# Kernel tuning notes

Hardware: AMD Instinct MI355X
Metric: run time of the kernel (lower is better)

## Reference

```python
import jax, jax.numpy as jnp
import numpy as np

N = 32768      # nodes
E = 262144     # edges (avg degree 8)
D = 128        # d_model (= per-head out_channels, concat=False)
H = 4          # heads
C = D          # out_channels per head
R = 64         # rel_dim (edge_dim)
NREL = 64      # n_rels
L = 2          # num_layers
LEAK = 0.2     # GATv2 leaky_relu slope
LN_EPS = 1e-5


def setup_inputs() -> dict:
    key = jax.random.key(0)
    ks = jax.random.split(key, 12)
    sdD = 1.0 / np.sqrt(D)
    sdR = 1.0 / np.sqrt(R)
    return {
        "x_flat": jax.random.normal(ks[0], (N, D), jnp.float32),
        "edge_index": jax.random.randint(ks[1], (2, E), 0, N, jnp.int64),
        "edge_type": jax.random.randint(ks[2], (E,), 0, NREL, jnp.int64),
        "valid_mask_flat": jnp.ones((N,), bool),
        "rel_emb": jax.random.normal(ks[3], (NREL, R), jnp.float32) * 0.1,
        "Wl": jax.random.normal(ks[4], (L, D, H * C), jnp.float32) * sdD,
        "bl": jnp.zeros((L, H * C), jnp.float32),
        "Wr": jax.random.normal(ks[5], (L, D, H * C), jnp.float32) * sdD,
        "br": jnp.zeros((L, H * C), jnp.float32),
        "We": jax.random.normal(ks[6], (L, R, H * C), jnp.float32) * sdR,
        "att": jax.random.normal(ks[7], (L, H, C), jnp.float32) * 0.1,
        "bias_o": jnp.zeros((L, D), jnp.float32),
        "ln_g": jnp.ones((L, D), jnp.float32),
        "ln_b": jnp.zeros((L, D), jnp.float32),
    }


def _gatv2_layer(h, src, dst, ea, Wl, bl, Wr, br, We, att, b):
    # h: [N,D]; src/dst: [E+N]; ea: [E+N,R] edge embeddings (incl. self loops)
    xl = (h @ Wl + bl).reshape(N, H, C)   # source transform
    xr = (h @ Wr + br).reshape(N, H, C)   # target transform
    ep = (ea @ We).reshape(-1, H, C)
    e = jax.nn.leaky_relu(xl[src] + xr[dst] + ep, LEAK)   # [E+N,H,C]
    logits = jnp.einsum('ehc,hc->eh', e, att)             # [E+N,H]
    # segment softmax over destination node
    m = jax.ops.segment_max(logits, dst, num_segments=N)
    m = jnp.where(jnp.isfinite(m), m, 0.0)
    p = jnp.exp(logits - m[dst])
    denom = jax.ops.segment_sum(p, dst, num_segments=N)
    alpha = p / (denom[dst] + 1e-16)                      # [E+N,H]
    out = jax.ops.segment_sum(alpha[:, :, None] * xl[src], dst, num_segments=N)
    return out.mean(axis=1) + b                           # concat=False -> head mean


def reference(x_flat, edge_index, edge_type, valid_mask_flat,
              rel_emb, Wl, bl, Wr, br, We, att, bias_o, ln_g, ln_b):
    x = jnp.where(valid_mask_flat[:, None], x_flat, 0.0)
    src, dst = edge_index[0], edge_index[1]
    ea = rel_emb[edge_type]                               # [E,R]
    # PyG add_self_loops with fill_value='mean': self-loop edge_attr is the
    # mean of incoming edge attrs per target node (0 if no incoming edges).
    ones = jnp.ones((E,), x.dtype)
    deg = jax.ops.segment_sum(ones, dst, num_segments=N)
    self_attr = jax.ops.segment_sum(ea, dst, num_segments=N) / jnp.maximum(deg, 1.0)[:, None]
    loop = jnp.arange(N, dtype=src.dtype)
    src_f = jnp.concatenate([src, loop])
    dst_f = jnp.concatenate([dst, loop])
    ea_f = jnp.concatenate([ea, self_attr], axis=0)

    h = x
    for l in range(L):
        msg = _gatv2_layer(h, src_f, dst_f, ea_f,
                           Wl[l], bl[l], Wr[l], br[l], We[l], att[l], bias_o[l])
        msg = jax.nn.gelu(msg, approximate=False)         # dropout = identity (eval)
        hn = h + msg
        mu = jnp.mean(hn, axis=-1, keepdims=True)
        var = jnp.mean(jnp.square(hn - mu), axis=-1, keepdims=True)
        h = (hn - mu) / jnp.sqrt(var + LN_EPS) * ln_g[l] + ln_b[l]
    return jnp.where(valid_mask_flat[:, None], h, 0.0)
```

## Files before the change

kernel.cpp:

```cpp
#include <hip/hip_runtime.h>
#include <hip/hip_bf16.h>
#include <math.h>

#define NN 32768
#define EE 262144
#define DM 128
#define HH 4
#define CC 128
#define HC 512
#define RD 64
#define NRELS 64
#define LEAKS 0.2f
#define LNEPS 1e-5f

typedef __hip_bfloat16 bf16;
typedef __attribute__((ext_vector_type(8))) short short8;
typedef __attribute__((ext_vector_type(4))) float f32x4;

__device__ __forceinline__ void unpack8(uint4 u, float* f) {
    f[0] = __uint_as_float((u.x & 0xffffu) << 16);
    f[1] = __uint_as_float(u.x & 0xffff0000u);
    f[2] = __uint_as_float((u.y & 0xffffu) << 16);
    f[3] = __uint_as_float(u.y & 0xffff0000u);
    f[4] = __uint_as_float((u.z & 0xffffu) << 16);
    f[5] = __uint_as_float(u.z & 0xffff0000u);
    f[6] = __uint_as_float((u.w & 0xffffu) << 16);
    f[7] = __uint_as_float(u.w & 0xffff0000u);
}

__global__ void k_deg(const int* __restrict__ dst, int* __restrict__ deg) {
    int e = blockIdx.x * 1024 + threadIdx.x;
    atomicAdd(&deg[dst[e]], 1);
}

__global__ void k_scan1(const int* __restrict__ deg, int* __restrict__ rowptr,
                        int* __restrict__ bsum) {
    __shared__ int s[256];
    int b = blockIdx.x, t = threadIdx.x;
    int v = deg[b * 256 + t];
    s[t] = v;
    __syncthreads();
    for (int off = 1; off < 256; off <<= 1) {
        int x = (t >= off) ? s[t - off] : 0;
        __syncthreads();
        s[t] += x;
        __syncthreads();
    }
    rowptr[b * 256 + t] = s[t] - v;
    if (t == 255) bsum[b] = s[255];
}

__global__ void k_small(const int* __restrict__ bsum, int* __restrict__ boff,
                        const int* __restrict__ hist, int* __restrict__ bcur) {
    __shared__ int s[128];
    int t = threadIdx.x;
    if (blockIdx.x == 0) {
        if (t < 128) {
            int v = bsum[t];
            s[t] = v;
        }
        __syncthreads();
        for (int off = 1; off < 128; off <<= 1) {
            int x = (t >= off && t < 128) ? s[t - off] : 0;
            __syncthreads();
            if (t < 128) s[t] += x;
            __syncthreads();
        }
        if (t < 128) boff[t] = s[t] - bsum[t];
        if (t == 127) boff[128] = s[127];
    } else {
        if (t < 64) s[t] = hist[t];
        __syncthreads();
        for (int off = 1; off < 64; off <<= 1) {
            int x = (t >= off && t < 64) ? s[t - off] : 0;
            __syncthreads();
            if (t < 64) s[t] += x;
            __syncthreads();
        }
        if (t < 64) bcur[t] = s[t] - hist[t];
    }
}

__global__ void k_s3p(int* __restrict__ rowptr, const int* __restrict__ boff,
                      const int* __restrict__ deg, int* __restrict__ bcur,
                      int* __restrict__ perm) {
    __shared__ int lh[64], lbase[64];
    int t = threadIdx.x;
    int i = blockIdx.x * 256 + t;
    rowptr[i] += boff[i >> 8];
    if (i == NN - 1) rowptr[NN] = boff[128];
    if (t < 64) lh[t] = 0;
    __syncthreads();
    int d = deg[i];
    int b = 63 - (d > 63 ? 63 : d);
    int my = atomicAdd(&lh[b], 1);
    __syncthreads();
    if (t < 64 && lh[t] > 0) lbase[t] = atomicAdd(&bcur[t], lh[t]);
    __syncthreads();
    perm[lbase[b] + my] = i;
}

__global__ void k_hist(const int* __restrict__ deg, int* __restrict__ hist) {
    __shared__ int lh[64];
    int t = threadIdx.x;
    if (t < 64) lh[t] = 0;
    __syncthreads();
    int d = deg[blockIdx.x * 256 + t];
    int b = 63 - (d > 63 ? 63 : d);
    atomicAdd(&lh[b], 1);
    __syncthreads();
    if (t < 64 && lh[t] > 0) atomicAdd(&hist[t], lh[t]);
}

__global__ void k_fill(const int* __restrict__ src, const int* __restrict__ dst,
                       const int* __restrict__ etype, const int* __restrict__ rowptr,
                       int* __restrict__ cursor, unsigned* __restrict__ csr) {
    int e = blockIdx.x * 1024 + threadIdx.x;
    int d = dst[e];
    int pos = atomicAdd(&cursor[d], 1);
    csr[rowptr[d] + pos] = (unsigned)src[e] | ((unsigned)etype[e] << 16);
}

__global__ void k_prep(const float* __restrict__ x, bf16* __restrict__ hb,
                       const float* __restrict__ Wl, const float* __restrict__ Wr,
                       bf16* __restrict__ Wt,
                       const float* __restrict__ rel_emb, const float* __restrict__ We,
                       bf16* __restrict__ wep) {
    __shared__ float sa[RD];
    int b = blockIdx.x, tid = threadIdx.x;
    if (b < 2048) {
        int i = b * 256 + tid;
        const float4* p = (const float4*)x;
        float4 f0 = p[i * 2], f1 = p[i * 2 + 1];
        bf16 o[8];
        o[0] = __float2bfloat16(f0.x); o[1] = __float2bfloat16(f0.y);
        o[2] = __float2bfloat16(f0.z); o[3] = __float2bfloat16(f0.w);
        o[4] = __float2bfloat16(f1.x); o[5] = __float2bfloat16(f1.y);
        o[6] = __float2bfloat16(f1.z); o[7] = __float2bfloat16(f1.w);
        *reinterpret_cast<uint4*>(hb + (size_t)i * 8) = *reinterpret_cast<uint4*>(o);
    } else if (b < 3072) {
        int idx = (b - 2048) * 256 + tid;
        int l = idx >> 17;
        int rem = idx & 131071;
        int k = rem >> 10;
        int c = rem & 1023;
        const float* WlL = Wl + (size_t)l * DM * HC;
        const float* WrL = Wr + (size_t)l * DM * HC;
        float v = (c < HC) ? WlL[k * HC + c] : WrL[k * HC + (c - HC)];
        Wt[(size_t)l * 1024 * DM + (size_t)c * DM + k] = __float2bfloat16(v);
    } else {
        int blk = b - 3072;
        int l = blk >> 6, r = blk & 63;
        const float* WeL = We + (size_t)l * RD * HC;
        if (tid < RD) sa[tid] = rel_emb[r * RD + tid];
        __syncthreads();
        for (int c = tid; c < HC; c += 256) {
            float s = 0.f;
#pragma unroll 8
            for (int k = 0; k < RD; ++k) s += sa[k] * WeL[k * HC + c];
            wep[(size_t)l * NRELS * HC + (size_t)r * HC + c] = __float2bfloat16(s);
        }
    }
}

__global__ __launch_bounds__(256) void k_gemm_mfma(
    const bf16* __restrict__ hb, const bf16* __restrict__ Wt,
    const float* __restrict__ bl, const float* __restrict__ br,
    bf16* __restrict__ xlb, bf16* __restrict__ xrb) {
    int lane = threadIdx.x & 63;
    int wave = threadIdx.x >> 6;
    int rbase = blockIdx.x * 32;
    int lr = lane & 15;
    int lk = lane >> 4;
    const short* ha = (const short*)hb;
    const short* wa = (const short*)Wt;

    short8 a[2][4];
#pragma unroll
    for (int mi = 0; mi < 2; ++mi)
#pragma unroll
        for (int kk = 0; kk < 4; ++kk)
            a[mi][kk] = *(const short8*)(ha + (size_t)(rbase + mi * 16 + lr) * DM + kk * 32 + lk * 8);

    for (int cg = 0; cg < 4; ++cg) {
        int cbase = cg * 256 + wave * 64;
        short8 b[4][4];
#pragma unroll
        for (int ni = 0; ni < 4; ++ni)
#pragma unroll
            for (int kk = 0; kk < 4; ++kk)
                b[ni][kk] = *(const short8*)(wa + (size_t)(cbase + ni * 16 + lr) * DM + kk * 32 + lk * 8);

        f32x4 c[2][4];
#pragma unroll
        for (int mi = 0; mi < 2; ++mi)
#pragma unroll
            for (int ni = 0; ni < 4; ++ni)
                c[mi][ni] = (f32x4){0.f, 0.f, 0.f, 0.f};

#pragma unroll
        for (int kk = 0; kk < 4; ++kk)
#pragma unroll
            for (int mi = 0; mi < 2; ++mi)
#pragma unroll
                for (int ni = 0; ni < 4; ++ni)
                    c[mi][ni] = __builtin_amdgcn_mfma_f32_16x16x32_bf16(
                        a[mi][kk], b[ni][kk], c[mi][ni], 0, 0, 0);

#pragma unroll
        for (int ni = 0; ni < 4; ++ni) {
            int col = cbase + ni * 16 + lr;
            float bv = (col < HC) ? bl[col] : br[col - HC];
            bf16* outp;
            int cc;
            if (col < HC) { outp = xlb; cc = col; } else { outp = xrb; cc = col - HC; }
#pragma unroll
            for (int mi = 0; mi < 2; ++mi) {
#pragma unroll
                for (int r = 0; r < 4; ++r) {
                    int row = rbase + mi * 16 + lk * 4 + r;
                    outp[(size_t)row * HC + cc] = __float2bfloat16(c[mi][ni][r] + bv);
                }
            }
        }
    }
}

__global__ void k_node(
    const bf16* __restrict__ xlb, const bf16* __restrict__ xrb,
    const bf16* __restrict__ wep,
    const unsigned* __restrict__ csr, const int* __restrict__ rowptr,
    const int* __restrict__ perm,
    const float* __restrict__ attL, const float* __restrict__ biasL,
    const float* __restrict__ lngL, const float* __restrict__ lnbL,
    const float* __restrict__ h_in, float* __restrict__ h_out,
    bf16* __restrict__ hb_out) {
    int tid = threadIdx.x;
    int lane = tid & 63;
    int wave = tid >> 6;
    int n = perm[blockIdx.x * 4 + wave];
    int head = lane >> 4;
    const int g0 = lane * 8;
    const int ch0 = (lane & 15) * 8;
    const short* xla = (const short*)xlb;
    const short* wpa = (const short*)wep;

    float attv[8];
#pragma unroll
    for (int j = 0; j < 8; ++j) attv[j] = attL[head * CC + ch0 + j];

    float xrn[8];
    unpack8(*(const uint4*)((const short*)xrb + (size_t)n * HC + g0), xrn);

    const float4* hp = (const float4*)(h_in + (size_t)n * DM + ch0);
    float4 h0 = hp[0], h1 = hp[1];

    float denom = 0.f;
    float acc[8], wpsum[8];
#pragma unroll
    for (int j = 0; j < 8; ++j) { acc[j] = 0.f; wpsum[j] = 0.f; }

    int r0 = rowptr[n], r1 = rowptr[n + 1];
    int d = r1 - r0;

    int i = r0;
    for (; i + 3 < r1; i += 4) {
        unsigned u0 = csr[i], u1 = csr[i + 1], u2 = csr[i + 2], u3 = csr[i + 3];
        uint4 xv0 = *(const uint4*)(xla + (size_t)(u0 & 0xffffu) * HC + g0);
        uint4 xv1 = *(const uint4*)(xla + (size_t)(u1 & 0xffffu) * HC + g0);
        uint4 xv2 = *(const uint4*)(xla + (size_t)(u2 & 0xffffu) * HC + g0);
        uint4 xv3 = *(const uint4*)(xla + (size_t)(u3 & 0xffffu) * HC + g0);
        uint4 wv0 = *(const uint4*)(wpa + (size_t)(u0 >> 16) * HC + g0);
        uint4 wv1 = *(const uint4*)(wpa + (size_t)(u1 >> 16) * HC + g0);
        uint4 wv2 = *(const uint4*)(wpa + (size_t)(u2 >> 16) * HC + g0);
        uint4 wv3 = *(const uint4*)(wpa + (size_t)(u3 >> 16) * HC + g0);
        float xs0[8], xs1[8], xs2[8], xs3[8];
        float w0[8], w1[8], w2[8], w3[8];
        unpack8(xv0, xs0); unpack8(xv1, xs1);
        unpack8(xv2, xs2); unpack8(xv3, xs3);
        unpack8(wv0, w0); unpack8(wv1, w1);
        unpack8(wv2, w2); unpack8(wv3, w3);
        float p0 = 0.f, p1 = 0.f, p2 = 0.f, p3 = 0.f;
#pragma unroll
        for (int j = 0; j < 8; ++j) {
            wpsum[j] += (w0[j] + w1[j]) + (w2[j] + w3[j]);
            float v0 = xs0[j] + xrn[j] + w0[j];
            v0 = (v0 > 0.f) ? v0 : LEAKS * v0;
            p0 += v0 * attv[j];
            float v1 = xs1[j] + xrn[j] + w1[j];
            v1 = (v1 > 0.f) ? v1 : LEAKS * v1;
            p1 += v1 * attv[j];
            float v2 = xs2[j] + xrn[j] + w2[j];
            v2 = (v2 > 0.f) ? v2 : LEAKS * v2;
            p2 += v2 * attv[j];
            float v3 = xs3[j] + xrn[j] + w3[j];
            v3 = (v3 > 0.f) ? v3 : LEAKS * v3;
            p3 += v3 * attv[j];
        }
        p0 += __shfl_xor(p0, 1); p1 += __shfl_xor(p1, 1);
        p2 += __shfl_xor(p2, 1); p3 += __shfl_xor(p3, 1);
        p0 += __shfl_xor(p0, 2); p1 += __shfl_xor(p1, 2);
        p2 += __shfl_xor(p2, 2); p3 += __shfl_xor(p3, 2);
        p0 += __shfl_xor(p0, 4); p1 += __shfl_xor(p1, 4);
        p2 += __shfl_xor(p2, 4); p3 += __shfl_xor(p3, 4);
        p0 += __shfl_xor(p0, 8); p1 += __shfl_xor(p1, 8);
        p2 += __shfl_xor(p2, 8); p3 += __shfl_xor(p3, 8);

        float e0 = __expf(fminf(p0, 80.f));
        float e1 = __expf(fminf(p1, 80.f));
        float e2 = __expf(fminf(p2, 80.f));
        float e3 = __expf(fminf(p3, 80.f));
        denom += (e0 + e1) + (e2 + e3);
#pragma unroll
        for (int j = 0; j < 8; ++j)
            acc[j] += (e0 * xs0[j] + e1 * xs1[j]) + (e2 * xs2[j] + e3 * xs3[j]);
    }
    for (; i < r1; ++i) {
        unsigned u = csr[i];
        uint4 xv = *(const uint4*)(xla + (size_t)(u & 0xffffu) * HC + g0);
        uint4 wv = *(const uint4*)(wpa + (size_t)(u >> 16) * HC + g0);
        float xs[8], wp[8];
        unpack8(xv, xs);
        unpack8(wv, wp);
        float p2 = 0.f;
#pragma unroll
        for (int j = 0; j < 8; ++j) {
            wpsum[j] += wp[j];
            float v = xs[j] + xrn[j] + wp[j];
            v = (v > 0.f) ? v : LEAKS * v;
            p2 += v * attv[j];
        }
        p2 += __shfl_xor(p2, 1);
        p2 += __shfl_xor(p2, 2);
        p2 += __shfl_xor(p2, 4);
        p2 += __shfl_xor(p2, 8);
        float pe = __expf(fminf(p2, 80.f));
        denom += pe;
#pragma unroll
        for (int j = 0; j < 8; ++j) acc[j] += pe * xs[j];
    }

    float xln[8];
    unpack8(*(const uint4*)(xla + (size_t)n * HC + g0), xln);
    float invd = (d > 0) ? (1.0f / (float)d) : 1.0f;
    float p2 = 0.f;
#pragma unroll
    for (int j = 0; j < 8; ++j) {
        float v = xln[j] + xrn[j] + wpsum[j] * invd;
        v = (v > 0.f) ? v : LEAKS * v;
        p2 += v * attv[j];
    }
    p2 += __shfl_xor(p2, 1);
    p2 += __shfl_xor(p2, 2);
    p2 += __shfl_xor(p2, 4);
    p2 += __shfl_xor(p2, 8);
    {
        float pe = __expf(fminf(p2, 80.f));
        denom += pe;
#pragma unroll
        for (int j = 0; j < 8; ++j) acc[j] += pe * xln[j];
    }

    float inv = 1.0f / (denom + 1e-16f);
    float hin[8] = {h0.x, h0.y, h0.z, h0.w, h1.x, h1.y, h1.z, h1.w};
    float hn[8];
    float lsum = 0.f, lsq = 0.f;
#pragma unroll
    for (int j = 0; j < 8; ++j) {
        float v = acc[j] * inv;
        v += __shfl_xor(v, 16);
        v += __shfl_xor(v, 32);
        float x = v * 0.25f + biasL[ch0 + j];
        float ge = 0.5f * x * (1.0f + erff(x * 0.70710678f));
        float hv = hin[j] + ge;
        hn[j] = hv;
        lsum += hv;
        lsq += hv * hv;
    }
    lsum += __shfl_xor(lsum, 1);
    lsum += __shfl_xor(lsum, 2);
    lsum += __shfl_xor(lsum, 4);
    lsum += __shfl_xor(lsum, 8);
    lsq += __shfl_xor(lsq, 1);
    lsq += __shfl_xor(lsq, 2);
    lsq += __shfl_xor(lsq, 4);
    lsq += __shfl_xor(lsq, 8);
    float mu = lsum * (1.0f / 128.f);
    float var = lsq * (1.0f / 128.f) - mu * mu;
    float rstd = rsqrtf(var + LNEPS);
    if (lane < 16) {
#pragma unroll
        for (int j = 0; j < 8; ++j) {
            float o = (hn[j] - mu) * rstd * lngL[ch0 + j] + lnbL[ch0 + j];
            h_out[(size_t)n * DM + ch0 + j] = o;
            if (hb_out) hb_out[(size_t)n * DM + ch0 + j] = __float2bfloat16(o);
        }
    }
}

extern "C" void kernel_launch(void* const* d_in, const int* in_sizes, int n_in,
                              void* d_out, int out_size, void* d_ws, size_t ws_size,
                              hipStream_t stream) {
    const float* x_flat   = (const float*)d_in[0];
    const int*   edge_idx = (const int*)d_in[1];
    const int*   edge_typ = (const int*)d_in[2];
    const float* rel_emb  = (const float*)d_in[4];
    const float* Wl       = (const float*)d_in[5];
    const float* bl       = (const float*)d_in[6];
    const float* Wr       = (const float*)d_in[7];
    const float* br       = (const float*)d_in[8];
    const float* We       = (const float*)d_in[9];
    const float* att      = (const float*)d_in[10];
    const float* bias_o   = (const float*)d_in[11];
    const float* ln_g     = (const float*)d_in[12];
    const float* ln_b     = (const float*)d_in[13];

    const int* srcp = edge_idx;
    const int* dstp = edge_idx + EE;

    char* w = (char*)d_ws;
    auto alloc = [&](size_t bytes) -> void* {
        void* p = (void*)w;
        w += (bytes + 255) & ~(size_t)255;
        return p;
    };
    bf16*  xlb    = (bf16*)alloc((size_t)NN * HC * 2);
    bf16*  xrb    = (bf16*)alloc((size_t)NN * HC * 2);
    bf16*  hb     = (bf16*)alloc((size_t)NN * DM * 2);
    float* h_mid  = (float*)alloc((size_t)NN * DM * 4);
    bf16*  wep    = (bf16*)alloc((size_t)2 * NRELS * HC * 2);
    bf16*  Wt     = (bf16*)alloc((size_t)2 * 1024 * DM * 2);
    int*   deg    = (int*)alloc((size_t)NN * 4);
    int*   cursor = (int*)alloc((size_t)NN * 4);
    int*   hist   = (int*)alloc((size_t)64 * 4);
    int*   bcur   = (int*)alloc((size_t)64 * 4);
    int*   rowptr = (int*)alloc((size_t)(NN + 1) * 4);
    int*   bsum   = (int*)alloc((size_t)128 * 4);
    int*   boff   = (int*)alloc((size_t)129 * 4);
    int*   perm   = (int*)alloc((size_t)NN * 4);
    unsigned* csr = (unsigned*)alloc((size_t)EE * 4);

    hipMemsetAsync(deg, 0, (size_t)NN * 8 + 512, stream);

    k_deg<<<EE / 1024, 1024, 0, stream>>>(dstp, deg);
    k_scan1<<<NN / 256, 256, 0, stream>>>(deg, rowptr, bsum);
    k_hist<<<NN / 256, 256, 0, stream>>>(deg, hist);
    k_small<<<2, 128, 0, stream>>>(bsum, boff, hist, bcur);
    k_s3p<<<NN / 256, 256, 0, stream>>>(rowptr, boff, deg, bcur, perm);
    k_fill<<<EE / 1024, 1024, 0, stream>>>(srcp, dstp, edge_typ, rowptr, cursor, csr);
    k_prep<<<3200, 256, 0, stream>>>(x_flat, hb, Wl, Wr, Wt, rel_emb, We, wep);

    const float* h = x_flat;
    for (int l = 0; l < 2; ++l) {
        k_gemm_mfma<<<NN / 32, 256, 0, stream>>>(
            hb, Wt + (size_t)l * 1024 * DM,
            bl + (size_t)l * HC, br + (size_t)l * HC, xlb, xrb);
        float* hout = (l == 0) ? h_mid : (float*)d_out;
        k_node<<<NN / 4, 256, 0, stream>>>(xlb, xrb, wep + (size_t)l * NRELS * HC,
                                           csr, rowptr, perm,
                                           att + (size_t)l * HH * CC,
                                           bias_o + (size_t)l * DM,
                                           ln_g + (size_t)l * DM,
                                           ln_b + (size_t)l * DM,
                                           h, hout, (l == 0) ? hb : (bf16*)nullptr);
        h = hout;
    }
}
```

Before: 451.0 us.

## Pipeline edge gathers into LDS ring via async global_load_lds in node kernel

Rewrites the per-node edge loop of k_node to stage each wave's CSR entries in shared memory and prefetch source-feature and edge-projection rows into a 4-deep LDS ring buffer using async global-to-LDS loads. Each iteration waits on an explicit vmcnt, reads the current slot, and issues the load for the edge four positions ahead. The goal is to hide gather latency while processing edges one at a time instead of in unrolled groups of four. It adds about 33KB of LDS per block, which may reduce occupancy, and relies on hand-written waitcnt values that must match the load count exactly. The h_in load is moved after the loop and the leaky-relu select becomes an fmax.

```diff
diff --git a/kernel.cpp b/kernel.cpp
--- a/kernel.cpp
+++ b/kernel.cpp
@@ -12,10 +12,18 @@
 #define NRELS 64
 #define LEAKS 0.2f
 #define LNEPS 1e-5f
+#define PIPE_L 4
 
 typedef __hip_bfloat16 bf16;
 typedef __attribute__((ext_vector_type(8))) short short8;
 typedef __attribute__((ext_vector_type(4))) float f32x4;
+
+typedef const __attribute__((address_space(1))) void* as1cv;
+typedef __attribute__((address_space(3))) void* as3v;
+
+__device__ __forceinline__ void gload16(const void* g, void* l) {
+    __builtin_amdgcn_global_load_lds((as1cv)g, (as3v)l, 16, 0, 0);
+}
 
 __device__ __forceinline__ void unpack8(uint4 u, float* f) {
     f[0] = __uint_as_float((u.x & 0xffffu) << 16);
@@ -55,10 +63,7 @@
     __shared__ int s[128];
     int t = threadIdx.x;
     if (blockIdx.x == 0) {
-        if (t < 128) {
-            int v = bsum[t];
-            s[t] = v;
-        }
+        if (t < 128) s[t] = bsum[t];
         __syncthreads();
         for (int off = 1; off < 128; off <<= 1) {
             int x = (t >= off && t < 128) ? s[t - off] : 0;
@@ -235,9 +240,14 @@
     const float* __restrict__ lngL, const float* __restrict__ lnbL,
     const float* __restrict__ h_in, float* __restrict__ h_out,
     bf16* __restrict__ hb_out) {
+    __shared__ uint4 smem[4 * 528];
     int tid = threadIdx.x;
     int lane = tid & 63;
     int wave = tid >> 6;
+    uint4* wls = smem + wave * 528;
+    unsigned* csrS = (unsigned*)wls;
+    unsigned char* ring = (unsigned char*)(wls + 16);
+
     int n = perm[blockIdx.x * 4 + wave];
     int head = lane >> 4;
     const int g0 = lane * 8;
@@ -245,78 +255,101 @@
     const short* xla = (const short*)xlb;
     const short* wpa = (const short*)wep;
 
+    int r0 = rowptr[n], r1 = rowptr[n + 1];
+    int d = r1 - r0;
+    int de = (d < 64) ? d : 64;
+
+    if (lane < de) csrS[lane] = csr[r0 + lane];
+
     float attv[8];
-#pragma unroll
-    for (int j = 0; j < 8; ++j) attv[j] = attL[head * CC + ch0 + j];
-
+    {
+        const float4* ap = (const float4*)(attL + head * CC + ch0);
+        float4 a0 = ap[0], a1 = ap[1];
+        attv[0] = a0.x; attv[1] = a0.y; attv[2] = a0.z; attv[3] = a0.w;
+        attv[4] = a1.x; attv[5] = a1.y; attv[6] = a1.z; attv[7] = a1.w;
+    }
     float xrn[8];
     unpack8(*(const uint4*)((const short*)xrb + (size_t)n * HC + g0), xrn);
 
-    const float4* hp = (const float4*)(h_in + (size_t)n * DM + ch0);
-    float4 h0 = hp[0], h1 = hp[1];
+    asm volatile("s_waitcnt vmcnt(0) lgkmcnt(0)" ::: "memory");
+    __builtin_amdgcn_sched_barrier(0);
 
     float denom = 0.f;
     float acc[8], wpsum[8];
 #pragma unroll
     for (int j = 0; j < 8; ++j) { acc[j] = 0.f; wpsum[j] = 0.f; }
 
-    int r0 = rowptr[n], r1 = rowptr[n + 1];
-    int d = r1 - r0;
-
-    int i = r0;
-    for (; i + 3 < r1; i += 4) {
-        unsigned u0 = csr[i], u1 = csr[i + 1], u2 = csr[i + 2], u3 = csr[i + 3];
-        uint4 xv0 = *(const uint4*)(xla + (size_t)(u0 & 0xffffu) * HC + g0);
-        uint4 xv1 = *(const uint4*)(xla + (size_t)(u1 & 0xffffu) * HC + g0);
-        uint4 xv2 = *(const uint4*)(xla + (size_t)(u2 & 0xffffu) * HC + g0);
-        uint4 xv3 = *(const uint4*)(xla + (size_t)(u3 & 0xffffu) * HC + g0);
-        uint4 wv0 = *(const uint4*)(wpa + (size_t)(u0 >> 16) * HC + g0);
-        uint4 wv1 = *(const uint4*)(wpa + (size_t)(u1 >> 16) * HC + g0);
-        uint4 wv2 = *(const uint4*)(wpa + (size_t)(u2 >> 16) * HC + g0);
-        uint4 wv3 = *(const uint4*)(wpa + (size_t)(u3 >> 16) * HC + g0);
-        float xs0[8], xs1[8], xs2[8], xs3[8];
-        float w0[8], w1[8], w2[8], w3[8];
-        unpack8(xv0, xs0); unpack8(xv1, xs1);
-        unpack8(xv2, xs2); unpack8(xv3, xs3);
-        unpack8(wv0, w0); unpack8(wv1, w1);
-        unpack8(wv2, w2); unpack8(wv3, w3);
-        float p0 = 0.f, p1 = 0.f, p2 = 0.f, p3 = 0.f;
+    int npre = (de < PIPE_L) ? de : PIPE_L;
+    for (int k = 0; k < npre; ++k) {
+        unsigned u = csrS[k];
+        unsigned char* slot = ring + (k & (PIPE_L - 1)) * 2048;
+        gload16(xla + (size_t)(u & 0xffffu) * HC + lane * 8, slot);
+        gload16(wpa + (size_t)(u >> 16) * HC + lane * 8, slot + 1024);
+    }
+
+    int i = 0;
+    for (; i + PIPE_L < de; ++i) {
+        asm volatile("s_waitcnt vmcnt(6)" ::: "memory");
+        __builtin_amdgcn_sched_barrier(0);
+        unsigned char* slot = ring + (i & (PIPE_L - 1)) * 2048;
+        uint4 xv = *(const uint4*)(slot + lane * 16);
+        uint4 wv = *(const uint4*)(slot + 1024 + lane * 16);
+        asm volatile("s_waitcnt lgkmcnt(0)" ::: "memory");
+        __builtin_amdgcn_sched_barrier(0);
+        {
+            unsigned u = csrS[i + PIPE_L];
+            gload16(xla + (size_t)(u & 0xffffu) * HC + lane * 8, slot);
+            gload16(wpa + (size_t)(u >> 16) * HC + lane * 8, slot + 1024);
+        }
+        float xs[8], wp[8];
+        unpack8(xv, xs);
+        unpack8(wv, wp);
+        float p2 = 0.f;
 #pragma unroll
         for (int j = 0; j < 8; ++j) {
-            wpsum[j] += (w0[j] + w1[j]) + (w2[j] + w3[j]);
-            float v0 = xs0[j] + xrn[j] + w0[j];
-            v0 = (v0 > 0.f) ? v0 : LEAKS * v0;
-            p0 += v0 * attv[j];
-            float v1 = xs1[j] + xrn[j] + w1[j];
-            v1 = (v1 > 0.f) ? v1 : LEAKS * v1;
-            p1 += v1 * attv[j];
-            float v2 = xs2[j] + xrn[j] + w2[j];
-            v2 = (v2 > 0.f) ? v2 : LEAKS * v2;
-            p2 += v2 * attv[j];
-            float v3 = xs3[j] + xrn[j] + w3[j];
-            v3 = (v3 > 0.f) ? v3 : LEAKS * v3;
-            p3 += v3 * attv[j];
-        }
-        p0 += __shfl_xor(p0, 1); p1 += __shfl_xor(p1, 1);
-        p2 += __shfl_xor(p2, 1); p3 += __shfl_xor(p3, 1);
-        p0 += __shfl_xor(p0, 2); p1 += __shfl_xor(p1, 2);
-        p2 += __shfl_xor(p2, 2); p3 += __shfl_xor(p3, 2);
-        p0 += __shfl_xor(p0, 4); p1 += __shfl_xor(p1, 4);
-        p2 += __shfl_xor(p2, 4); p3 += __shfl_xor(p3, 4);
-        p0 += __shfl_xor(p0, 8); p1 += __shfl_xor(p1, 8);
-        p2 += __shfl_xor(p2, 8); p3 += __shfl_xor(p3, 8);
-
-        float e0 = __expf(fminf(p0, 80.f));
-        float e1 = __expf(fminf(p1, 80.f));
-        float e2 = __expf(fminf(p2, 80.f));
-        float e3 = __expf(fminf(p3, 80.f));
-        denom += (e0 + e1) + (e2 + e3);
-#pragma unroll
-        for (int j = 0; j < 8; ++j)
-            acc[j] += (e0 * xs0[j] + e1 * xs1[j]) + (e2 * xs2[j] + e3 * xs3[j]);
-    }
-    for (; i < r1; ++i) {
-        unsigned u = csr[i];
+            wpsum[j] += wp[j];
+            float v = xs[j] + xrn[j] + wp[j];
+            v = fmaxf(v, LEAKS * v);
+            p2 += v * attv[j];
+        }
+        p2 += __shfl_xor(p2, 1);
+        p2 += __shfl_xor(p2, 2);
+        p2 += __shfl_xor(p2, 4);
+        p2 += __shfl_xor(p2, 8);
+        float pe = __expf(fminf(p2, 80.f));
+        denom += pe;
+#pragma unroll
+        for (int j = 0; j < 8; ++j) acc[j] += pe * xs[j];
+    }
+    asm volatile("s_waitcnt vmcnt(0)" ::: "memory");
+    __builtin_amdgcn_sched_barrier(0);
+    for (; i < de; ++i) {
+        unsigned char* slot = ring + (i & (PIPE_L - 1)) * 2048;
+        uint4 xv = *(const uint4*)(slot + lane * 16);
+        uint4 wv = *(const uint4*)(slot + 1024 + lane * 16);
+        float xs[8], wp[8];
+        unpack8(xv, xs);
+        unpack8(wv, wp);
+        float p2 = 0.f;
+#pragma unroll
+        for (int j = 0; j < 8; ++j) {
+            wpsum[j] += wp[j];
+            float v = xs[j] + xrn[j] + wp[j];
+            v = fmaxf(v, LEAKS * v);
+            p2 += v * attv[j];
+        }
+        p2 += __shfl_xor(p2, 1);
+        p2 += __shfl_xor(p2, 2);
+        p2 += __shfl_xor(p2, 4);
+        p2 += __shfl_xor(p2, 8);
+        float pe = __expf(fminf(p2, 80.f));
+        denom += pe;
+#pragma unroll
+        for (int j = 0; j < 8; ++j) acc[j] += pe * xs[j];
+    }
+
+    for (int k = 64; k < d; ++k) {
+        unsigned u = csr[r0 + k];
         uint4 xv = *(const uint4*)(xla + (size_t)(u & 0xffffu) * HC + g0);
         uint4 wv = *(const uint4*)(wpa + (size_t)(u >> 16) * HC + g0);
         float xs[8], wp[8];
@@ -327,7 +360,7 @@
         for (int j = 0; j < 8; ++j) {
             wpsum[j] += wp[j];
             float v = xs[j] + xrn[j] + wp[j];
-            v = (v > 0.f) ? v : LEAKS * v;
+            v = fmaxf(v, LEAKS * v);
             p2 += v * attv[j];
         }
         p2 += __shfl_xor(p2, 1);
@@ -347,7 +380,7 @@
 #pragma unroll
     for (int j = 0; j < 8; ++j) {
         float v = xln[j] + xrn[j] + wpsum[j] * invd;
-        v = (v > 0.f) ? v : LEAKS * v;
+        v = fmaxf(v, LEAKS * v);
         p2 += v * attv[j];
     }
     p2 += __shfl_xor(p2, 1);
@@ -362,6 +395,8 @@
     }
 
     float inv = 1.0f / (denom + 1e-16f);
+    const float4* hp = (const float4*)(h_in + (size_t)n * DM + ch0);
+    float4 h0 = hp[0], h1 = hp[1];
     float hin[8] = {h0.x, h0.y, h0.z, h0.w, h1.x, h1.y, h1.z, h1.w};
     float hn[8];
     float lsum = 0.f, lsq = 0.f;
```

Result: faster. 425.0 us (-5.8%).
